# Performance work log

Measured on AMD Instinct MI355X. Metric: run time of the kernel, lower is better.

The kernel has to match this reference:

```python
import jax, jax.numpy as jnp
import numpy as np

N_NODES = 50000
N_EDGES = 600000
IN_C, HID, OUT_C, HEADS = 128, 64, 16, 4


def setup_inputs() -> dict:
    key = jax.random.key(0)
    ks = jax.random.split(key, 12)
    s = 1.0 / np.sqrt(HID)
    return {
        "x": jax.random.normal(ks[0], (N_NODES, IN_C), dtype=jnp.float32),
        "edge_index": jax.random.randint(ks[1], (2, N_EDGES), 0, N_NODES, dtype=jnp.int64),
        "W_lin": jax.random.normal(ks[2], (IN_C, HID), dtype=jnp.float32) / np.sqrt(IN_C),
        "b_lin": jnp.zeros((HID,), dtype=jnp.float32),
        "Wq": jax.random.normal(ks[3], (HID, HID), dtype=jnp.float32) * s,
        "bq": jnp.zeros((HID,), dtype=jnp.float32),
        "Wk": jax.random.normal(ks[4], (HID, HID), dtype=jnp.float32) * s,
        "bk": jnp.zeros((HID,), dtype=jnp.float32),
        "Wv": jax.random.normal(ks[5], (HID, HID), dtype=jnp.float32) * s,
        "bv": jnp.zeros((HID,), dtype=jnp.float32),
        "W_out": jax.random.normal(ks[6], (HID, OUT_C), dtype=jnp.float32) * s,
        "b_out": jnp.zeros((OUT_C,), dtype=jnp.float32),
    }


def _dna_conv(xs, src, dst, norm, Wq, bq, Wk, bk, Wv, bv):
    # xs: [N, L, C] stacked layer histories. Multi-head attention per edge:
    # query = target node's latest layer, keys/values = source node's full history.
    N, L, C = xs.shape
    d = C // HEADS
    q = (xs[:, -1] @ Wq + bq).reshape(N, HEADS, d)          # [N,H,d]
    k = (xs @ Wk + bk).reshape(N, L, HEADS, d)               # [N,L,H,d]
    v = (xs @ Wv + bv).reshape(N, L, HEADS, d)
    scores = jnp.einsum('ehd,elhd->ehl', q[dst], k[src]) / jnp.sqrt(jnp.float32(d))
    attn = jax.nn.softmax(scores, axis=-1)                   # softmax over layer history
    msg = jnp.einsum('ehl,elhd->ehd', attn, v[src]).reshape(-1, C)  # [E,C]
    msg = msg * norm[:, None]                                # GCN symmetric norm
    return jax.ops.segment_sum(msg, dst, num_segments=N)


def reference(x, edge_index, W_lin, b_lin, Wq, bq, Wk, bk, Wv, bv, W_out, b_out):
    N = x.shape[0]
    loop = jnp.arange(N, dtype=edge_index.dtype)
    src = jnp.concatenate([edge_index[0], loop])
    dst = jnp.concatenate([edge_index[1], loop])
    deg = jax.ops.segment_sum(jnp.ones_like(dst, dtype=x.dtype), dst, num_segments=N)
    dinv = jnp.where(deg > 0, jax.lax.rsqrt(jnp.maximum(deg, 1.0)), 0.0)
    norm = dinv[src] * dinv[dst]

    h = x @ W_lin + b_lin                                    # [N,HID]
    xs = h[:, None, :]
    for _ in range(3):
        out = _dna_conv(xs, src, dst, norm, Wq, bq, Wk, bk, Wv, bv)
        xs = jnp.concatenate([xs, out[:, None, :]], axis=1)
    return xs[:, -1] @ W_out + b_out                          # [N,OUT_C]
```

## Files before the change

kernel.cpp:

```cpp
#include <hip/hip_runtime.h>


__device__ inline unsigned short bf16_rne(float f) {
    unsigned int u = __float_as_uint(f);
    unsigned int r = u + 0x7FFFu + ((u >> 16) & 1u);
    return (unsigned short)(r >> 16);
}
__device__ inline float kf(unsigned int u) { return __uint_as_float(u << 16); }
__device__ inline float vf(unsigned int u) { return __uint_as_float(u & 0xFFFF0000u); }

__global__ __launch_bounds__(256) void hist_dst_k(const int* __restrict__ dst,
                                                  int* __restrict__ cnt, int E) {
    int e = blockIdx.x * 256 + threadIdx.x;
    if (e < E) atomicAdd(&cnt[dst[e]], 1);
}

__global__ __launch_bounds__(256) void scan1_k(const int* __restrict__ cnt,
                                               int* __restrict__ excl,
                                               int* __restrict__ aux,
                                               float* __restrict__ dinv, int N) {
    __shared__ int wtot[4];
    int b = blockIdx.x, t = threadIdx.x;
    int lane = t & 63, w = t >> 6;
    int base = b * 1024 + t * 4;
    int v0 = (base + 0 < N) ? cnt[base + 0] + 1 : 0;
    int v1 = (base + 1 < N) ? cnt[base + 1] + 1 : 0;
    int v2 = (base + 2 < N) ? cnt[base + 2] + 1 : 0;
    int v3 = (base + 3 < N) ? cnt[base + 3] + 1 : 0;
    if (base + 0 < N) dinv[base + 0] = rsqrtf((float)v0);
    if (base + 1 < N) dinv[base + 1] = rsqrtf((float)v1);
    if (base + 2 < N) dinv[base + 2] = rsqrtf((float)v2);
    if (base + 3 < N) dinv[base + 3] = rsqrtf((float)v3);
    int s = v0 + v1 + v2 + v3;
    int incl = s;
#pragma unroll
    for (int off = 1; off < 64; off <<= 1) {
        int u = __shfl_up(incl, off);
        if (lane >= off) incl += u;
    }
    if (lane == 63) wtot[w] = incl;
    __syncthreads();
    int wb = 0;
#pragma unroll
    for (int j = 0; j < 4; ++j) if (j < w) wb += wtot[j];
    int ex = wb + incl - s;
    if (base + 0 < N) excl[base + 0] = ex;
    if (base + 1 < N) excl[base + 1] = ex + v0;
    if (base + 2 < N) excl[base + 2] = ex + v0 + v1;
    if (base + 3 < N) excl[base + 3] = ex + v0 + v1 + v2;
    if (t == 0) aux[b] = wtot[0] + wtot[1] + wtot[2] + wtot[3];
}

__global__ __launch_bounds__(256) void scan_add2_k(int* __restrict__ offs,
                                                   const int* __restrict__ aux,
                                                   const int* __restrict__ cnt,
                                                   int* __restrict__ cursor,
                                                   int N, int nb) {
    int i = blockIdx.x * 256 + threadIdx.x;
    int c = blockIdx.x >> 2;
    int lane = threadIdx.x & 63;
    int v = (lane < c && lane < nb) ? aux[lane] : 0;
#pragma unroll
    for (int off = 32; off >= 1; off >>= 1) v += __shfl_xor(v, off);
    if (i < N) {
        int o = offs[i] + v;
        offs[i] = o;
        cursor[i] = o;
        if (i == N - 1) offs[N] = o + cnt[i] + 1;
    }
}

__global__ __launch_bounds__(256) void scatter_dst_k(const int* __restrict__ src,
                                                     const int* __restrict__ dst,
                                                     int* __restrict__ cursor,
                                                     int* __restrict__ src_sorted,
                                                     int E, int N) {
    int e = blockIdx.x * 256 + threadIdx.x;
    int M = E + N;
    if (e >= M) return;
    int s, d;
    if (e < E) { s = src[e]; d = dst[e]; }
    else       { s = d = e - E; }
    int pos = atomicAdd(&cursor[d], 1);
    src_sorted[pos] = s;
}

__global__ __launch_bounds__(256) void lin128_64_k(const float* __restrict__ x,
                                                   const float* __restrict__ W,
                                                   const float* __restrict__ b,
                                                   float* __restrict__ y, int N) {
    __shared__ float sW[128 * 64];
    __shared__ float sb[64];
    for (int i = threadIdx.x; i < 128 * 64; i += 256) sW[i] = W[i];
    if (threadIdx.x < 64) sb[threadIdx.x] = b[threadIdx.x];
    __syncthreads();
    int w = threadIdx.x >> 6, c = threadIdx.x & 63;
    int r0 = blockIdx.x * 16 + w * 4;
    if (r0 >= N) return;
    const float* xr[4];
#pragma unroll
    for (int j = 0; j < 4; ++j) {
        int r = r0 + j; if (r > N - 1) r = N - 1;
        xr[j] = x + (size_t)r * 128;
    }
    float acc[4];
#pragma unroll
    for (int j = 0; j < 4; ++j) acc[j] = sb[c];
    for (int k = 0; k < 128; ++k) {
        float wv = sW[k * 64 + c];
#pragma unroll
        for (int j = 0; j < 4; ++j) acc[j] = fmaf(xr[j][k], wv, acc[j]);
    }
#pragma unroll
    for (int j = 0; j < 4; ++j) {
        int r = r0 + j;
        if (r < N) y[(size_t)r * 64 + c] = acc[j];
    }
}

template <bool WRITE_V0>
__global__ __launch_bounds__(192) void proj_qkv_k(const float* __restrict__ X,
                                                  const float* __restrict__ Wq, const float* __restrict__ bq,
                                                  const float* __restrict__ Wk, const float* __restrict__ bk,
                                                  const float* __restrict__ Wv, const float* __restrict__ bv,
                                                  const float* __restrict__ dinv,
                                                  float* __restrict__ q,
                                                  unsigned int* __restrict__ PL,
                                                  unsigned short* __restrict__ V0,
                                                  int N, int l, int RPB) {
    int w = threadIdx.x >> 6;
    int c = threadIdx.x & 63;
    const float* W = (w == 0) ? Wq : (w == 1) ? Wk : Wv;
    const float* B = (w == 0) ? bq : (w == 1) ? bk : bv;
    float wr[64];
#pragma unroll
    for (int k = 0; k < 64; ++k) wr[k] = W[k * 64 + c];
    float bias = B[c];
    int r0 = blockIdx.x * RPB;
    int r1 = r0 + RPB; if (r1 > N) r1 = N;
    unsigned short* PLh = (unsigned short*)PL;
    for (int r = r0; r < r1; ++r) {
        float xv = X[(size_t)r * 64 + c];
        float a = bias;
#pragma unroll
        for (int k = 0; k < 64; ++k) {
            float xk = __int_as_float(__builtin_amdgcn_readlane(__float_as_int(xv), k));
            a = fmaf(xk, wr[k], a);
        }
        if (w == 0) {
            q[(size_t)r * 64 + c] = a * 0.25f;
        } else if (w == 1) {
            PLh[((size_t)r * 192 + l * 64 + c) * 2] = bf16_rne(a);
        } else {
            unsigned short vb = bf16_rne(a * dinv[r]);
            PLh[((size_t)r * 192 + l * 64 + c) * 2 + 1] = vb;
            if (WRITE_V0) V0[(size_t)r * 64 + c] = vb;
        }
    }
}

template <int L, bool EMIT_OUT>
__global__ __launch_bounds__(256) void attn_g16_k(const int* __restrict__ offs,
                                                  const int* __restrict__ src_sorted,
                                                  const float* __restrict__ dinv,
                                                  const float* __restrict__ q,
                                                  const unsigned int* __restrict__ PL,
                                                  const unsigned short* __restrict__ V0,
                                                  const float* __restrict__ Wo,
                                                  const float* __restrict__ bo,
                                                  float* __restrict__ outv,
                                                  int N) {
    constexpr int LDSN = EMIT_OUT ? (16 * 68 + 64 * 16 + 16) : 1;
    __shared__ float lds[LDSN];
    float* rowS = lds;
    float* sWo  = lds + 16 * 68;
    float* sbo  = sWo + 64 * 16;
    if (EMIT_OUT) {
        for (int i = threadIdx.x; i < 64 * 16; i += 256) sWo[i] = Wo[i];
        if (threadIdx.x < 16) sbo[threadIdx.x] = bo[threadIdx.x];
    }

    int d  = (blockIdx.x * 256 + threadIdx.x) >> 4;
    int gl = threadIdx.x & 15;
    int gb = threadIdx.x & 48;
    float a0 = 0.f, a1 = 0.f, a2 = 0.f, a3 = 0.f;
    float dv = 0.f;

    if (d < N) {
        dv = dinv[d];
        int beg = offs[d], end = offs[d + 1];
        float4 qv = make_float4(0.f, 0.f, 0.f, 0.f);
        if (L > 1) qv = *(const float4*)(q + (size_t)d * 64 + gl * 4);

        for (int base = beg; base < end; base += 16) {
            int m = end - base;
            if (m > 16) m = 16;
            int sid = (base + gl < end) ? src_sorted[base + gl] : 0;
            int mm1 = m - 1;
#define SIDAT(j) __shfl(sid, gb + ((j) < mm1 ? (j) : mm1))
            uint4 A0, A1, A2, B0, B1, B2, C0, C1, C2;
            uint2 Av, Bv, Cv;
            int sA = SIDAT(0), sB = SIDAT(1);
            if (L == 1) {
                Av = *(const uint2*)(V0 + (size_t)sA * 64 + gl * 4);
                Bv = *(const uint2*)(V0 + (size_t)sB * 64 + gl * 4);
            } else {
                const uint4* pa = (const uint4*)(PL + (size_t)sA * 192) + gl;
                A0 = pa[0]; A1 = pa[16]; if (L > 2) A2 = pa[32];
                const uint4* pb = (const uint4*)(PL + (size_t)sB * 192) + gl;
                B0 = pb[0]; B1 = pb[16]; if (L > 2) B2 = pb[32];
            }

            for (int i = 0; i < m; ++i) {
                int sC = SIDAT(i + 2);
                if (L == 1) {
                    Cv = *(const uint2*)(V0 + (size_t)sC * 64 + gl * 4);
                } else {
                    const uint4* pc = (const uint4*)(PL + (size_t)sC * 192) + gl;
                    C0 = pc[0]; C1 = pc[16]; if (L > 2) C2 = pc[32];
                }

                if (L == 1) {
                    a0 += __uint_as_float((Av.x & 0xFFFFu) << 16);
                    a1 += __uint_as_float(Av.x & 0xFFFF0000u);
                    a2 += __uint_as_float((Av.y & 0xFFFFu) << 16);
                    a3 += __uint_as_float(Av.y & 0xFFFF0000u);
                } else {
                    float p0 = qv.x * kf(A0.x);
                    p0 = fmaf(qv.y, kf(A0.y), p0);
                    p0 = fmaf(qv.z, kf(A0.z), p0);
                    p0 = fmaf(qv.w, kf(A0.w), p0);
                    float p1 = qv.x * kf(A1.x);
                    p1 = fmaf(qv.y, kf(A1.y), p1);
                    p1 = fmaf(qv.z, kf(A1.z), p1);
                    p1 = fmaf(qv.w, kf(A1.w), p1);
                    float p2 = 0.f;
                    if (L > 2) {
                        p2 = qv.x * kf(A2.x);
                        p2 = fmaf(qv.y, kf(A2.y), p2);
                        p2 = fmaf(qv.z, kf(A2.z), p2);
                        p2 = fmaf(qv.w, kf(A2.w), p2);
                    }
                    p0 += __shfl_xor(p0, 1); p0 += __shfl_xor(p0, 2);
                    p1 += __shfl_xor(p1, 1); p1 += __shfl_xor(p1, 2);
                    if (L > 2) { p2 += __shfl_xor(p2, 1); p2 += __shfl_xor(p2, 2); }
                    float w0, w1, w2 = 0.f;
                    if (L == 2) {
                        float e = __expf(p1 - p0);
                        w0 = __builtin_amdgcn_rcpf(1.0f + e);
                        w1 = 1.0f - w0;
                    } else {
                        float mx = fmaxf(fmaxf(p0, p1), p2);
                        float e0 = __expf(p0 - mx);
                        float e1 = __expf(p1 - mx);
                        float e2 = __expf(p2 - mx);
                        float inv = __builtin_amdgcn_rcpf(e0 + e1 + e2);
                        w0 = e0 * inv; w1 = e1 * inv; w2 = e2 * inv;
                    }
                    a0 = fmaf(w0, vf(A0.x), a0);
                    a1 = fmaf(w0, vf(A0.y), a1);
                    a2 = fmaf(w0, vf(A0.z), a2);
                    a3 = fmaf(w0, vf(A0.w), a3);
                    a0 = fmaf(w1, vf(A1.x), a0);
                    a1 = fmaf(w1, vf(A1.y), a1);
                    a2 = fmaf(w1, vf(A1.z), a2);
                    a3 = fmaf(w1, vf(A1.w), a3);
                    if (L > 2) {
                        a0 = fmaf(w2, vf(A2.x), a0);
                        a1 = fmaf(w2, vf(A2.y), a1);
                        a2 = fmaf(w2, vf(A2.z), a2);
                        a3 = fmaf(w2, vf(A2.w), a3);
                    }
                }
                if (L == 1) {
                    Av = Bv; Bv = Cv;
                } else {
                    A0 = B0; A1 = B1; B0 = C0; B1 = C1;
                    if (L > 2) { A2 = B2; B2 = C2; }
                }
            }
#undef SIDAT
        }
    }

    if (EMIT_OUT) {
        int w16 = threadIdx.x >> 4;
        if (d < N) {
            rowS[w16 * 68 + gl * 4 + 0] = a0 * dv;
            rowS[w16 * 68 + gl * 4 + 1] = a1 * dv;
            rowS[w16 * 68 + gl * 4 + 2] = a2 * dv;
            rowS[w16 * 68 + gl * 4 + 3] = a3 * dv;
        }
        __syncthreads();
        int node = threadIdx.x >> 4;
        int co   = threadIdx.x & 15;
        int dn   = blockIdx.x * 16 + node;
        if (dn < N) {
            float acc = sbo[co];
#pragma unroll 16
            for (int k = 0; k < 64; ++k)
                acc = fmaf(rowS[node * 68 + k], sWo[k * 16 + co], acc);
            outv[(size_t)dn * 16 + co] = acc;
        }
    } else {
        if (d < N)
            *(float4*)(outv + (size_t)d * 64 + gl * 4) =
                make_float4(a0 * dv, a1 * dv, a2 * dv, a3 * dv);
    }
}

extern "C" void kernel_launch(void* const* d_in, const int* in_sizes, int n_in,
                              void* d_out, int out_size, void* d_ws, size_t ws_size,
                              hipStream_t stream) {
    const float* x     = (const float*)d_in[0];
    const int*   ei    = (const int*)d_in[1];
    const float* W_lin = (const float*)d_in[2];
    const float* b_lin = (const float*)d_in[3];
    const float* Wq    = (const float*)d_in[4];
    const float* bq    = (const float*)d_in[5];
    const float* Wk    = (const float*)d_in[6];
    const float* bk    = (const float*)d_in[7];
    const float* Wv    = (const float*)d_in[8];
    const float* bv    = (const float*)d_in[9];
    const float* W_out = (const float*)d_in[10];
    const float* b_out = (const float*)d_in[11];
    float* out = (float*)d_out;

    const int N = in_sizes[0] / 128;
    const int E = in_sizes[1] / 2;
    const int M = E + N;
    const int* srcp = ei;
    const int* dstp = ei + E;

    char* wsb = (char*)d_ws;
    float*          dinv       = (float*)wsb;           wsb += (size_t)N * sizeof(float);
    int*            cnt        = (int*)wsb;             wsb += (size_t)N * sizeof(int);
    int*            offs       = (int*)wsb;             wsb += (size_t)(N + 1) * sizeof(int);
    int*            cursor     = (int*)wsb;             wsb += (size_t)N * sizeof(int);
    int*            aux        = (int*)wsb;             wsb += 64 * sizeof(int);
    int*            src_sorted = (int*)wsb;             wsb += (size_t)M * sizeof(int);
    float*          qb         = (float*)wsb;           wsb += (size_t)N * 64 * sizeof(float);
    unsigned int*   PL         = (unsigned int*)wsb;    wsb += (size_t)N * 192 * sizeof(unsigned int);
    unsigned short* V0p        = (unsigned short*)wsb;  wsb += (size_t)N * 64 * sizeof(unsigned short);
    float*          hA         = (float*)wsb;           wsb += (size_t)N * 64 * sizeof(float);
    float*          outb       = (float*)wsb;

    const int gN   = (N + 255) / 256;
    const int gE   = (E + 255) / 256;
    const int gM   = (M + 255) / 256;
    const int g16  = (N + 15) / 16;
    const int nb   = (N + 1023) / 1024;
    const int RPB  = 16;
    const int gP   = (N + RPB - 1) / RPB;

    hipMemsetAsync(cnt, 0, (size_t)N * sizeof(int), stream);
    hist_dst_k<<<gE, 256, 0, stream>>>(dstp, cnt, E);
    scan1_k<<<nb, 256, 0, stream>>>(cnt, offs, aux, dinv, N);
    scan_add2_k<<<gN, 256, 0, stream>>>(offs, aux, cnt, cursor, N, nb);
    scatter_dst_k<<<gM, 256, 0, stream>>>(srcp, dstp, cursor, src_sorted, E, N);

    lin128_64_k<<<g16, 256, 0, stream>>>(x, W_lin, b_lin, hA, N);
    proj_qkv_k<true><<<gP, 192, 0, stream>>>(hA, Wq, bq, Wk, bk, Wv, bv, dinv,
                                             qb, PL, V0p, N, 0, RPB);

    attn_g16_k<1, false><<<g16, 256, 0, stream>>>(offs, src_sorted, dinv, qb, PL, V0p,
                                                  nullptr, nullptr, outb, N);
    proj_qkv_k<false><<<gP, 192, 0, stream>>>(outb, Wq, bq, Wk, bk, Wv, bv, dinv,
                                              qb, PL, V0p, N, 1, RPB);
    attn_g16_k<2, false><<<g16, 256, 0, stream>>>(offs, src_sorted, dinv, qb, PL, V0p,
                                                  nullptr, nullptr, outb, N);
    proj_qkv_k<false><<<gP, 192, 0, stream>>>(outb, Wq, bq, Wk, bk, Wv, bv, dinv,
                                              qb, PL, V0p, N, 2, RPB);
    attn_g16_k<3, true><<<g16, 256, 0, stream>>>(offs, src_sorted, dinv, qb, PL, V0p,
                                                 W_out, b_out, out, N);
}
```

Before: 430.9 us.

## Assign one wavefront per destination node with four edge groups in parallel

```diff
diff --git a/kernel.cpp b/kernel.cpp
--- a/kernel.cpp
+++ b/kernel.cpp
@@ -160,7 +160,7 @@
 }
 
 template <int L, bool EMIT_OUT>
-__global__ __launch_bounds__(256) void attn_g16_k(const int* __restrict__ offs,
+__global__ __launch_bounds__(256) void attn_w64_k(const int* __restrict__ offs,
                                                   const int* __restrict__ src_sorted,
                                                   const float* __restrict__ dinv,
                                                   const float* __restrict__ q,
@@ -170,61 +170,61 @@
                                                   const float* __restrict__ bo,
                                                   float* __restrict__ outv,
                                                   int N) {
-    constexpr int LDSN = EMIT_OUT ? (16 * 68 + 64 * 16 + 16) : 1;
+    constexpr int LDSN = EMIT_OUT ? (4 * 68 + 64 * 16 + 16) : 1;
     __shared__ float lds[LDSN];
     float* rowS = lds;
-    float* sWo  = lds + 16 * 68;
+    float* sWo  = lds + 4 * 68;
     float* sbo  = sWo + 64 * 16;
     if (EMIT_OUT) {
         for (int i = threadIdx.x; i < 64 * 16; i += 256) sWo[i] = Wo[i];
         if (threadIdx.x < 16) sbo[threadIdx.x] = bo[threadIdx.x];
     }
 
-    int d  = (blockIdx.x * 256 + threadIdx.x) >> 4;
-    int gl = threadIdx.x & 15;
-    int gb = threadIdx.x & 48;
+    int wv   = threadIdx.x >> 6;
+    int lane = threadIdx.x & 63;
+    int gl   = lane & 15;
+    int eg   = lane >> 4;
+    int d    = blockIdx.x * 4 + wv;
+
     float a0 = 0.f, a1 = 0.f, a2 = 0.f, a3 = 0.f;
-    float dv = 0.f;
 
     if (d < N) {
-        dv = dinv[d];
         int beg = offs[d], end = offs[d + 1];
         float4 qv = make_float4(0.f, 0.f, 0.f, 0.f);
         if (L > 1) qv = *(const float4*)(q + (size_t)d * 64 + gl * 4);
 
-        for (int base = beg; base < end; base += 16) {
+        for (int base = beg; base < end; base += 64) {
             int m = end - base;
-            if (m > 16) m = 16;
-            int sid = (base + gl < end) ? src_sorted[base + gl] : 0;
+            if (m > 64) m = 64;
+            int sid = (base + lane < end) ? src_sorted[base + lane] : 0;
+            int nit = (m + 3) >> 2;
             int mm1 = m - 1;
-#define SIDAT(j) __shfl(sid, gb + ((j) < mm1 ? (j) : mm1))
-            uint4 A0, A1, A2, B0, B1, B2, C0, C1, C2;
-            uint2 Av, Bv, Cv;
-            int sA = SIDAT(0), sB = SIDAT(1);
+
+            int idx = eg; if (idx > mm1) idx = mm1;
+            int sA = __shfl(sid, idx);
+            uint4 A0, A1, A2, B0, B1, B2;
+            uint2 Av, Bv;
             if (L == 1) {
                 Av = *(const uint2*)(V0 + (size_t)sA * 64 + gl * 4);
-                Bv = *(const uint2*)(V0 + (size_t)sB * 64 + gl * 4);
             } else {
                 const uint4* pa = (const uint4*)(PL + (size_t)sA * 192) + gl;
                 A0 = pa[0]; A1 = pa[16]; if (L > 2) A2 = pa[32];
-                const uint4* pb = (const uint4*)(PL + (size_t)sB * 192) + gl;
-                B0 = pb[0]; B1 = pb[16]; if (L > 2) B2 = pb[32];
             }
 
-            for (int i = 0; i < m; ++i) {
-                int sC = SIDAT(i + 2);
+            for (int i = 0; i < nit; ++i) {
+                int nidx = (i + 1) * 4 + eg; if (nidx > mm1) nidx = mm1;
+                int sB = __shfl(sid, nidx);
                 if (L == 1) {
-                    Cv = *(const uint2*)(V0 + (size_t)sC * 64 + gl * 4);
+                    Bv = *(const uint2*)(V0 + (size_t)sB * 64 + gl * 4);
                 } else {
-                    const uint4* pc = (const uint4*)(PL + (size_t)sC * 192) + gl;
-                    C0 = pc[0]; C1 = pc[16]; if (L > 2) C2 = pc[32];
+                    const uint4* pb = (const uint4*)(PL + (size_t)sB * 192) + gl;
+                    B0 = pb[0]; B1 = pb[16]; if (L > 2) B2 = pb[32];
                 }
 
+                float vm = ((i * 4 + eg) <= mm1) ? 1.f : 0.f;
                 if (L == 1) {
-                    a0 += __uint_as_float((Av.x & 0xFFFFu) << 16);
-                    a1 += __uint_as_float(Av.x & 0xFFFF0000u);
-                    a2 += __uint_as_float((Av.y & 0xFFFFu) << 16);
-                    a3 += __uint_as_float(Av.y & 0xFFFF0000u);
+                    a0 += vm * kf(Av.x); a1 += vm * vf(Av.x);
+                    a2 += vm * kf(Av.y); a3 += vm * vf(Av.y);
                 } else {
                     float p0 = qv.x * kf(A0.x);
                     p0 = fmaf(qv.y, kf(A0.y), p0);
@@ -257,6 +257,7 @@
                         float inv = __builtin_amdgcn_rcpf(e0 + e1 + e2);
                         w0 = e0 * inv; w1 = e1 * inv; w2 = e2 * inv;
                     }
+                    w0 *= vm; w1 *= vm; if (L > 2) w2 *= vm;
                     a0 = fmaf(w0, vf(A0.x), a0);
                     a1 = fmaf(w0, vf(A0.y), a1);
                     a2 = fmaf(w0, vf(A0.z), a2);
@@ -273,39 +274,46 @@
                     }
                 }
                 if (L == 1) {
-                    Av = Bv; Bv = Cv;
+                    Av = Bv;
                 } else {
-                    A0 = B0; A1 = B1; B0 = C0; B1 = C1;
-                    if (L > 2) { A2 = B2; B2 = C2; }
+                    A0 = B0; A1 = B1;
+                    if (L > 2) A2 = B2;
                 }
             }
-#undef SIDAT
-        }
+        }
+
+        a0 += __shfl_xor(a0, 16); a0 += __shfl_xor(a0, 32);
+        a1 += __shfl_xor(a1, 16); a1 += __shfl_xor(a1, 32);
+        a2 += __shfl_xor(a2, 16); a2 += __shfl_xor(a2, 32);
+        a3 += __shfl_xor(a3, 16); a3 += __shfl_xor(a3, 32);
+        float dv = dinv[d];
+        a0 *= dv; a1 *= dv; a2 *= dv; a3 *= dv;
     }
 
     if (EMIT_OUT) {
-        int w16 = threadIdx.x >> 4;
-        if (d < N) {
-            rowS[w16 * 68 + gl * 4 + 0] = a0 * dv;
-            rowS[w16 * 68 + gl * 4 + 1] = a1 * dv;
-            rowS[w16 * 68 + gl * 4 + 2] = a2 * dv;
-            rowS[w16 * 68 + gl * 4 + 3] = a3 * dv;
+        if (d < N && eg == 0) {
+            rowS[wv * 68 + gl * 4 + 0] = a0;
+            rowS[wv * 68 + gl * 4 + 1] = a1;
+            rowS[wv * 68 + gl * 4 + 2] = a2;
+            rowS[wv * 68 + gl * 4 + 3] = a3;
         }
         __syncthreads();
-        int node = threadIdx.x >> 4;
-        int co   = threadIdx.x & 15;
-        int dn   = blockIdx.x * 16 + node;
-        if (dn < N) {
-            float acc = sbo[co];
+        if (threadIdx.x < 64) {
+            int node = threadIdx.x >> 4;
+            int co   = threadIdx.x & 15;
+            int dn   = blockIdx.x * 4 + node;
+            if (dn < N) {
+                float acc = sbo[co];
 #pragma unroll 16
-            for (int k = 0; k < 64; ++k)
-                acc = fmaf(rowS[node * 68 + k], sWo[k * 16 + co], acc);
-            outv[(size_t)dn * 16 + co] = acc;
+                for (int k = 0; k < 64; ++k)
+                    acc = fmaf(rowS[node * 68 + k], sWo[k * 16 + co], acc);
+                outv[(size_t)dn * 16 + co] = acc;
+            }
         }
     } else {
-        if (d < N)
+        if (d < N && eg == 0)
             *(float4*)(outv + (size_t)d * 64 + gl * 4) =
-                make_float4(a0 * dv, a1 * dv, a2 * dv, a3 * dv);
+                make_float4(a0, a1, a2, a3);
     }
 }
 
@@ -349,6 +357,7 @@
     const int gE   = (E + 255) / 256;
     const int gM   = (M + 255) / 256;
     const int g16  = (N + 15) / 16;
+    const int gA4  = (N + 3) / 4;
     const int nb   = (N + 1023) / 1024;
     const int RPB  = 16;
     const int gP   = (N + RPB - 1) / RPB;
@@ -363,14 +372,14 @@
     proj_qkv_k<true><<<gP, 192, 0, stream>>>(hA, Wq, bq, Wk, bk, Wv, bv, dinv,
                                              qb, PL, V0p, N, 0, RPB);
 
-    attn_g16_k<1, false><<<g16, 256, 0, stream>>>(offs, src_sorted, dinv, qb, PL, V0p,
+    attn_w64_k<1, false><<<gA4, 256, 0, stream>>>(offs, src_sorted, dinv, qb, PL, V0p,
                                                   nullptr, nullptr, outb, N);
     proj_qkv_k<false><<<gP, 192, 0, stream>>>(outb, Wq, bq, Wk, bk, Wv, bv, dinv,
                                               qb, PL, V0p, N, 1, RPB);
-    attn_g16_k<2, false><<<g16, 256, 0, stream>>>(offs, src_sorted, dinv, qb, PL, V0p,
+    attn_w64_k<2, false><<<gA4, 256, 0, stream>>>(offs, src_sorted, dinv, qb, PL, V0p,
                                                   nullptr, nullptr, outb, N);
     proj_qkv_k<false><<<gP, 192, 0, stream>>>(outb, Wq, bq, Wk, bk, Wv, bv, dinv,
                                               qb, PL, V0p, N, 2, RPB);
-    attn_g16_k<3, true><<<g16, 256, 0, stream>>>(offs, src_sorted, dinv, qb, PL, V0p,
+    attn_w64_k<3, true><<<gA4, 256, 0, stream>>>(offs, src_sorted, dinv, qb, PL, V0p,
                                                  W_out, b_out, out, N);
 }
```

New measurement: 422.0 us. 1.02x faster.
